# Optimization experiments

Hardware: AMD Instinct MI355X
Metric: run time of the kernel (lower is better)

Reference implementation:

```python
import jax, jax.numpy as jnp
import numpy as np

RADIUS = 0.25  # module init arg


def _spp(x):
    """Spatial pyramid max pooling over the (K=8, C) plane.
    x: [B, N, 8, C] -> [B, N, 21] (4x4 + 2x2 + 1x1 bins)."""
    B, N, K, C = x.shape
    outs = []
    for h, w in ((4, 4), (2, 2), (1, 1)):
        r = x.reshape(B, N, h, K // h, w, C // w)
        outs.append(r.max(axis=(3, 5)).reshape(B, N, h * w))
    return jnp.concatenate(outs, axis=-1)


def _pointsift_select(xyz, radius):
    """Octant-wise nearest-neighbor selection. xyz: [Bp, N, 3] -> idx [Bp, N, 8]."""
    Bp, N, _ = xyz.shape
    judge = radius * radius
    # diff[b, n, m] = xyz[b, m] - xyz[b, n]  (point m relative to centroid n)
    diff = xyz[:, None, :, :] - xyz[:, :, None, :]          # [Bp, N, N, 3]
    dist = jnp.sum(diff * diff, axis=-1)                     # [Bp, N, N]
    octw = jnp.array([4, 2, 1], dtype=jnp.int32)
    sub = jnp.sum((diff + 1.0).astype(jnp.int32) * octw, -1)  # [Bp, N, N] octant id
    valid = (dist > 1e-10) & (dist < judge)
    eye = jnp.eye(N, dtype=bool)                             # self entry gets judge_dist
    idxs = []
    for i in range(8):
        d_i = jnp.where(valid & (sub == i), dist, 1e10)
        d_i = jnp.where(eye, judge, d_i)
        idxs.append(jnp.argmin(d_i, axis=-1))                # first-min, matches torch
    return jnp.stack(idxs, axis=-1)                          # [Bp, N, 8]


def setup_inputs() -> dict:
    key = jax.random.key(0)
    ks = jax.random.split(key, 7)
    C = 256
    x = jax.random.uniform(ks[0], (2, 2, 2048, 3), dtype=jnp.float32)
    w1 = jax.random.normal(ks[1], (C, 3), dtype=jnp.float32) * 0.05
    b1 = jax.random.normal(ks[2], (C,), dtype=jnp.float32) * 0.05
    w2 = jax.random.normal(ks[3], (C, C), dtype=jnp.float32) * 0.05
    b2 = jax.random.normal(ks[4], (C,), dtype=jnp.float32) * 0.05
    w3 = jax.random.normal(ks[5], (C, C), dtype=jnp.float32) * 0.05
    b3 = jax.random.normal(ks[6], (C,), dtype=jnp.float32) * 0.05
    return {"x": x, "w1": w1, "b1": b1, "w2": w2, "b2": b2, "w3": w3, "b3": b3}


def reference(x, w1, b1, w2, b2, w3, b3):
    B, T, N, _ = x.shape
    xyz = x.reshape(B * T, N, 3)
    idx = _pointsift_select(xyz, RADIUS)                     # [Bp, N, 8]
    b_idx = jnp.arange(B * T)[:, None, None]
    grouped = xyz[b_idx, idx] - xyz[:, :, None, :]           # [Bp, N, 8, 3] relative coords
    # three stacked 1x1 convs (no nonlinearity, per original Sequential)
    h = jnp.einsum('bnkc,oc->bnko', grouped, w1) + b1
    h = jnp.einsum('bnkc,oc->bnko', h, w2) + b2
    h = jnp.einsum('bnkc,oc->bnko', h, w3) + b3              # [Bp, N, 8, C]
    out = _spp(h)                                            # [Bp, N, 21]
    return out.reshape(B, T, N, -1)
```

## Files before the change

### kernel.cpp

```cpp
#include <hip/hip_runtime.h>

#define NPTS 2048
#define CCH  256

template <int CTRL>
__device__ __forceinline__ float dppf(float v) {
    return __int_as_float(__builtin_amdgcn_update_dpp(
        0, __float_as_int(v), CTRL, 0xF, 0xF, true));
}
__device__ __forceinline__ float row16_max(float v) {
    v = fmaxf(v, dppf<0xB1>(v));
    v = fmaxf(v, dppf<0x4E>(v));
    v = fmaxf(v, dppf<0x141>(v));
    v = fmaxf(v, dppf<0x140>(v));
    return v;
}
__device__ __forceinline__ float row16_sum(float v) {
    v += dppf<0xB1>(v);
    v += dppf<0x4E>(v);
    v += dppf<0x141>(v);
    v += dppf<0x140>(v);
    return v;
}
__device__ __forceinline__ float wave_sum(float v) {
    v = row16_sum(v);
    v += __shfl_xor(v, 16, 64);
    v += __shfl_xor(v, 32, 64);
    return v;
}

__device__ __forceinline__ int cell_coord(float v) {
    int c = (int)(v * 4.0f);
    return min(3, max(0, c));
}


__global__ __launch_bounds__(256) void prep_kernel(
    const float* __restrict__ w1, const float* __restrict__ b1,
    const float* __restrict__ w2, const float* __restrict__ b2,
    const float* __restrict__ w3, const float* __restrict__ b3,
    float* __restrict__ ws)
{
    __shared__ float  w3row[2][CCH];
    __shared__ float4 wpart[2][4];
    int o0 = blockIdx.x * 2, c = threadIdx.x;

    float w3c0 = w3[(o0 + 0) * CCH + c];
    float w3c1 = w3[(o0 + 1) * CCH + c];
    w3row[0][c] = w3c0;
    w3row[1][c] = w3c1;
    __syncthreads();

    float a0 = 0.f, a1 = 0.f, a2 = 0.f, a3 = 0.f;
    float b0 = 0.f, b1p = 0.f, b2p = 0.f, b3p = 0.f;
    const float* w2c = w2 + c;
    for (int k = 0; k < CCH; k += 4) {
        float q0 = w2c[(k + 0) * CCH];
        float q1 = w2c[(k + 1) * CCH];
        float q2 = w2c[(k + 2) * CCH];
        float q3 = w2c[(k + 3) * CCH];
        a0 = fmaf(w3row[0][k + 0], q0, a0);
        a1 = fmaf(w3row[0][k + 1], q1, a1);
        a2 = fmaf(w3row[0][k + 2], q2, a2);
        a3 = fmaf(w3row[0][k + 3], q3, a3);
        b0  = fmaf(w3row[1][k + 0], q0, b0);
        b1p = fmaf(w3row[1][k + 1], q1, b1p);
        b2p = fmaf(w3row[1][k + 2], q2, b2p);
        b3p = fmaf(w3row[1][k + 3], q3, b3p);
    }
    float accA = (a0 + a1) + (a2 + a3);
    float accB = (b0 + b1p) + (b2p + b3p);

    float w1x = w1[c * 3 + 0], w1y = w1[c * 3 + 1], w1z = w1[c * 3 + 2];
    float b1c = b1[c], b2c = b2[c];

    float4 vA = make_float4(accA * w1x, accA * w1y, accA * w1z,
                            fmaf(accA, b1c, w3c0 * b2c));
    float4 vB = make_float4(accB * w1x, accB * w1y, accB * w1z,
                            fmaf(accB, b1c, w3c1 * b2c));
    vA.x = wave_sum(vA.x); vA.y = wave_sum(vA.y);
    vA.z = wave_sum(vA.z); vA.w = wave_sum(vA.w);
    vB.x = wave_sum(vB.x); vB.y = wave_sum(vB.y);
    vB.z = wave_sum(vB.z); vB.w = wave_sum(vB.w);
    if ((c & 63) == 0) {
        wpart[0][c >> 6] = vA;
        wpart[1][c >> 6] = vB;
    }
    __syncthreads();
    if (c < 2) {
        int o = o0 + c;
        float4 p0 = wpart[c][0], p1 = wpart[c][1], p2 = wpart[c][2], p3 = wpart[c][3];
        ws[o * 3 + 0] = (p0.x + p1.x) + (p2.x + p3.x);
        ws[o * 3 + 1] = (p0.y + p1.y) + (p2.y + p3.y);
        ws[o * 3 + 2] = (p0.z + p1.z) + (p2.z + p3.z);
        ws[3 * CCH + o] = (p0.w + p1.w) + (p2.w + p3.w) + b3[o];
    }
}

__global__ __launch_bounds__(1024) void pointsift_kernel(
    const float* __restrict__ x,
    const float* __restrict__ ws,
    float* __restrict__ out)
{
    __shared__ float4 scrd[NPTS];
    __shared__ unsigned sstart[66];
    __shared__ unsigned shist[64];
    __shared__ unsigned scur[64];
    __shared__ unsigned long long soct[16][8];

    int tid = threadIdx.x;
    int batch = blockIdx.x >> 7;
    int n0    = (blockIdx.x & 127) * 16;
    const float* xb = x + (size_t)batch * NPTS * 3;

    if (tid < 64) shist[tid] = 0;
    __syncthreads();

    float2 f0 = *(const float2*)(xb + 6 * tid + 0);
    float2 f1 = *(const float2*)(xb + 6 * tid + 2);
    float2 f2 = *(const float2*)(xb + 6 * tid + 4);
    float3 p0 = make_float3(f0.x, f0.y, f1.x);
    float3 p1 = make_float3(f1.y, f2.x, f2.y);
    int c0 = (cell_coord(p0.x) << 4) | (cell_coord(p0.y) << 2) | cell_coord(p0.z);
    int c1 = (cell_coord(p1.x) << 4) | (cell_coord(p1.y) << 2) | cell_coord(p1.z);
    atomicAdd(&shist[c0], 1u);
    atomicAdd(&shist[c1], 1u);
    __syncthreads();

    if (tid < 64) {
        unsigned v = shist[tid];
        unsigned incl = v;
#pragma unroll
        for (int s = 1; s < 64; s <<= 1) {
            unsigned o = __shfl_up(incl, s, 64);
            if (tid >= s) incl += o;
        }
        unsigned excl = incl - v;
        sstart[tid] = excl;
        scur[tid] = excl;
        if (tid == 63) sstart[64] = NPTS;
    }
    __syncthreads();

    {
        unsigned q0 = atomicAdd(&scur[c0], 1u);
        scrd[q0] = make_float4(p0.x, p0.y, p0.z, __uint_as_float(2u * tid));
        unsigned q1 = atomicAdd(&scur[c1], 1u);
        scrd[q1] = make_float4(p1.x, p1.y, p1.z, __uint_as_float(2u * tid + 1u));
    }

    int wave = tid >> 6;
    int lane = tid & 63;
    int n = n0 + wave;

    float3 cpt = *(const float3*)(xb + 3 * n);
    float cx = cpt.x, cy = cpt.y, cz = cpt.z;

    if (lane < 8)
        soct[wave][lane] = (0x7f800000ULL << 32) | (unsigned)n;

    __syncthreads();

    int ccx = cell_coord(cx), ccy = cell_coord(cy), ccz = cell_coord(cz);
    int zlo = ccz > 0 ? ccz - 1 : 0;
    int zhi = ccz < 3 ? ccz + 1 : 3;

    for (int di = -1; di <= 1; ++di) {
        int a = ccx + di;
        if ((unsigned)a > 3u) continue;
        for (int dj = -1; dj <= 1; ++dj) {
            int bc = ccy + dj;
            if ((unsigned)bc > 3u) continue;
            int base = (a << 4) | (bc << 2);
            unsigned s0 = sstart[base + zlo];
            unsigned e0 = sstart[base + zhi + 1];
            for (unsigned pp = s0 + lane; pp < e0; pp += 64) {
                float4 p = scrd[pp];
                float dx = p.x - cx, dy = p.y - cy, dz = p.z - cz;
                float d2 = __fadd_rn(__fadd_rn(__fmul_rn(dx, dx), __fmul_rn(dy, dy)),
                                     __fmul_rn(dz, dz));
                if ((d2 > 1e-10f) && (d2 < 0.0625f)) {
                    int oct = 4 * (int)(dx + 1.0f) + 2 * (int)(dy + 1.0f) + (int)(dz + 1.0f);
                    unsigned long long key =
                        ((unsigned long long)__float_as_uint(d2) << 32) |
                        __float_as_uint(p.w);
                    __hip_atomic_fetch_min(&soct[wave][oct], key,
                                           __ATOMIC_RELAXED,
                                           __HIP_MEMORY_SCOPE_WORKGROUP);
                }
            }
        }
    }

    int nidx[8];
#pragma unroll
    for (int k = 0; k < 8; ++k)
        nidx[k] = (int)(unsigned)soct[wave][k];

    const float4* wsv = (const float4*)ws;
    float4 wa = wsv[lane * 3 + 0];
    float4 wb = wsv[lane * 3 + 1];
    float4 wc = wsv[lane * 3 + 2];
    float4 be = ((const float4*)(ws + 3 * CCH))[lane];
    float w[4][3] = {{wa.x, wa.y, wa.z}, {wa.w, wb.x, wb.y},
                     {wb.z, wb.w, wc.x}, {wc.y, wc.z, wc.w}};
    float bev[4] = {be.x, be.y, be.z, be.w};

    float m16[4];
#pragma unroll
    for (int i = 0; i < 4; ++i) m16[i] = -__builtin_inff();
#pragma unroll
    for (int k = 0; k < 8; ++k) {
        float3 p = *(const float3*)(xb + 3 * nidx[k]);
        float gx = p.x - cx, gy = p.y - cy, gz = p.z - cz;
#pragma unroll
        for (int q = 0; q < 4; ++q) {
            float h = fmaf(gx, w[q][0], fmaf(gy, w[q][1], fmaf(gz, w[q][2], bev[q])));
            m16[k >> 1] = fmaxf(m16[k >> 1], h);
        }
    }

    float t[4], u[4];
#pragma unroll
    for (int i = 0; i < 4; ++i) {
        m16[i] = row16_max(m16[i]);
        t[i] = fmaxf(m16[i], __shfl_xor(m16[i], 16, 64));
        u[i] = fmaxf(t[i], __shfl_xor(t[i], 32, 64));
    }

    float* op = out + ((size_t)batch * NPTS + n) * 21;
    if ((lane & 15) == 0) {
        int j = lane >> 4;
#pragma unroll
        for (int i = 0; i < 4; ++i)
            op[i * 4 + j] = m16[i];
    }
    if (lane == 0 || lane == 32) {
        int j2 = lane >> 5;
        op[16 + 0 * 2 + j2] = fmaxf(t[0], t[1]);
        op[16 + 1 * 2 + j2] = fmaxf(t[2], t[3]);
    }
    if (lane == 0) {
        op[20] = fmaxf(fmaxf(u[0], u[1]), fmaxf(u[2], u[3]));
    }
}

extern "C" void kernel_launch(void* const* d_in, const int* in_sizes, int n_in,
                              void* d_out, int out_size, void* d_ws, size_t ws_size,
                              hipStream_t stream) {
    const float* x  = (const float*)d_in[0];
    const float* w1 = (const float*)d_in[1];
    const float* b1 = (const float*)d_in[2];
    const float* w2 = (const float*)d_in[3];
    const float* b2 = (const float*)d_in[4];
    const float* w3 = (const float*)d_in[5];
    const float* b3 = (const float*)d_in[6];
    float* out = (float*)d_out;
    float* ws  = (float*)d_ws;

    prep_kernel<<<CCH / 2, CCH, 0, stream>>>(w1, b1, w2, b2, w3, b3, ws);

    int Bp = in_sizes[0] / (NPTS * 3);
    pointsift_kernel<<<Bp * (NPTS / 16), 1024, 0, stream>>>(x, ws, out);
}
```

Before: 22.15 us.

## Hoist per-batch spatial bucket sort into prep kernel, shrink search blocks

Moves the per-batch grid histogram and counting sort out of every search block and into extra blocks of the prep kernel. The sorted coordinates and cell offsets now go to the workspace, so each search block no longer repeats the 2048-point sort in LDS. Search blocks drop from 1024 threads and 16 centroids to 256 threads and 4 centroids, with a launch-bounds occupancy hint. Neighbor reads now come from global or L2 memory instead of LDS, and the batch index is taken from the low bits of the block index, which assumes Bp==4.

Result: slower. 22.66 us (+2.3%).

```diff
diff --git a/kernel.cpp b/kernel.cpp
--- a/kernel.cpp
+++ b/kernel.cpp
@@ -2,6 +2,9 @@
 
 #define NPTS 2048
 #define CCH  256
+
+#define STARTS_OFF 4096
+#define CRD_OFF    8192
 
 template <int CTRL>
 __device__ __forceinline__ float dppf(float v) {
@@ -34,120 +37,138 @@
     return min(3, max(0, c));
 }
 
-
-__global__ __launch_bounds__(256) void prep_kernel(
+__global__ __launch_bounds__(256) void prep_sort_kernel(
+    const float* __restrict__ x,
     const float* __restrict__ w1, const float* __restrict__ b1,
     const float* __restrict__ w2, const float* __restrict__ b2,
     const float* __restrict__ w3, const float* __restrict__ b3,
-    float* __restrict__ ws)
+    float* __restrict__ ws, int Bp)
 {
     __shared__ float  w3row[2][CCH];
     __shared__ float4 wpart[2][4];
-    int o0 = blockIdx.x * 2, c = threadIdx.x;
-
-    float w3c0 = w3[(o0 + 0) * CCH + c];
-    float w3c1 = w3[(o0 + 1) * CCH + c];
-    w3row[0][c] = w3c0;
-    w3row[1][c] = w3c1;
-    __syncthreads();
-
-    float a0 = 0.f, a1 = 0.f, a2 = 0.f, a3 = 0.f;
-    float b0 = 0.f, b1p = 0.f, b2p = 0.f, b3p = 0.f;
-    const float* w2c = w2 + c;
-    for (int k = 0; k < CCH; k += 4) {
-        float q0 = w2c[(k + 0) * CCH];
-        float q1 = w2c[(k + 1) * CCH];
-        float q2 = w2c[(k + 2) * CCH];
-        float q3 = w2c[(k + 3) * CCH];
-        a0 = fmaf(w3row[0][k + 0], q0, a0);
-        a1 = fmaf(w3row[0][k + 1], q1, a1);
-        a2 = fmaf(w3row[0][k + 2], q2, a2);
-        a3 = fmaf(w3row[0][k + 3], q3, a3);
-        b0  = fmaf(w3row[1][k + 0], q0, b0);
-        b1p = fmaf(w3row[1][k + 1], q1, b1p);
-        b2p = fmaf(w3row[1][k + 2], q2, b2p);
-        b3p = fmaf(w3row[1][k + 3], q3, b3p);
-    }
-    float accA = (a0 + a1) + (a2 + a3);
-    float accB = (b0 + b1p) + (b2p + b3p);
-
-    float w1x = w1[c * 3 + 0], w1y = w1[c * 3 + 1], w1z = w1[c * 3 + 2];
-    float b1c = b1[c], b2c = b2[c];
-
-    float4 vA = make_float4(accA * w1x, accA * w1y, accA * w1z,
-                            fmaf(accA, b1c, w3c0 * b2c));
-    float4 vB = make_float4(accB * w1x, accB * w1y, accB * w1z,
-                            fmaf(accB, b1c, w3c1 * b2c));
-    vA.x = wave_sum(vA.x); vA.y = wave_sum(vA.y);
-    vA.z = wave_sum(vA.z); vA.w = wave_sum(vA.w);
-    vB.x = wave_sum(vB.x); vB.y = wave_sum(vB.y);
-    vB.z = wave_sum(vB.z); vB.w = wave_sum(vB.w);
-    if ((c & 63) == 0) {
-        wpart[0][c >> 6] = vA;
-        wpart[1][c >> 6] = vB;
-    }
-    __syncthreads();
-    if (c < 2) {
-        int o = o0 + c;
-        float4 p0 = wpart[c][0], p1 = wpart[c][1], p2 = wpart[c][2], p3 = wpart[c][3];
-        ws[o * 3 + 0] = (p0.x + p1.x) + (p2.x + p3.x);
-        ws[o * 3 + 1] = (p0.y + p1.y) + (p2.y + p3.y);
-        ws[o * 3 + 2] = (p0.z + p1.z) + (p2.z + p3.z);
-        ws[3 * CCH + o] = (p0.w + p1.w) + (p2.w + p3.w) + b3[o];
-    }
-}
-
-__global__ __launch_bounds__(1024) void pointsift_kernel(
+    __shared__ unsigned shist[64];
+    __shared__ unsigned scur[64];
+
+    int tid = threadIdx.x;
+
+    if ((int)blockIdx.x < CCH / 2) {
+        int o0 = blockIdx.x * 2, c = tid;
+        float w3c0 = w3[(o0 + 0) * CCH + c];
+        float w3c1 = w3[(o0 + 1) * CCH + c];
+        w3row[0][c] = w3c0;
+        w3row[1][c] = w3c1;
+        __syncthreads();
+
+        float a0 = 0.f, a1 = 0.f, a2 = 0.f, a3 = 0.f;
+        float b0 = 0.f, b1p = 0.f, b2p = 0.f, b3p = 0.f;
+        const float* w2c = w2 + c;
+        for (int k = 0; k < CCH; k += 4) {
+            float q0 = w2c[(k + 0) * CCH];
+            float q1 = w2c[(k + 1) * CCH];
+            float q2 = w2c[(k + 2) * CCH];
+            float q3 = w2c[(k + 3) * CCH];
+            a0 = fmaf(w3row[0][k + 0], q0, a0);
+            a1 = fmaf(w3row[0][k + 1], q1, a1);
+            a2 = fmaf(w3row[0][k + 2], q2, a2);
+            a3 = fmaf(w3row[0][k + 3], q3, a3);
+            b0  = fmaf(w3row[1][k + 0], q0, b0);
+            b1p = fmaf(w3row[1][k + 1], q1, b1p);
+            b2p = fmaf(w3row[1][k + 2], q2, b2p);
+            b3p = fmaf(w3row[1][k + 3], q3, b3p);
+        }
+        float accA = (a0 + a1) + (a2 + a3);
+        float accB = (b0 + b1p) + (b2p + b3p);
+
+        float w1x = w1[c * 3 + 0], w1y = w1[c * 3 + 1], w1z = w1[c * 3 + 2];
+        float b1c = b1[c], b2c = b2[c];
+
+        float4 vA = make_float4(accA * w1x, accA * w1y, accA * w1z,
+                                fmaf(accA, b1c, w3c0 * b2c));
+        float4 vB = make_float4(accB * w1x, accB * w1y, accB * w1z,
+                                fmaf(accB, b1c, w3c1 * b2c));
+        vA.x = wave_sum(vA.x); vA.y = wave_sum(vA.y);
+        vA.z = wave_sum(vA.z); vA.w = wave_sum(vA.w);
+        vB.x = wave_sum(vB.x); vB.y = wave_sum(vB.y);
+        vB.z = wave_sum(vB.z); vB.w = wave_sum(vB.w);
+        if ((c & 63) == 0) {
+            wpart[0][c >> 6] = vA;
+            wpart[1][c >> 6] = vB;
+        }
+        __syncthreads();
+        if (c < 2) {
+            int o = o0 + c;
+            float4 p0 = wpart[c][0], p1 = wpart[c][1], p2 = wpart[c][2], p3 = wpart[c][3];
+            ws[o * 3 + 0] = (p0.x + p1.x) + (p2.x + p3.x);
+            ws[o * 3 + 1] = (p0.y + p1.y) + (p2.y + p3.y);
+            ws[o * 3 + 2] = (p0.z + p1.z) + (p2.z + p3.z);
+            ws[3 * CCH + o] = (p0.w + p1.w) + (p2.w + p3.w) + b3[o];
+        }
+        return;
+    }
+
+    int b = blockIdx.x - CCH / 2;
+    if (b >= Bp) return;
+    const float* xb = x + (size_t)b * NPTS * 3;
+
+    if (tid < 64) shist[tid] = 0;
+    __syncthreads();
+
+    float a[24];
+#pragma unroll
+    for (int j = 0; j < 6; ++j)
+        *(float4*)(a + 4 * j) = ((const float4*)xb)[tid * 6 + j];
+
+    int cl[8];
+#pragma unroll
+    for (int k = 0; k < 8; ++k) {
+        cl[k] = (cell_coord(a[3 * k + 0]) << 4) |
+                (cell_coord(a[3 * k + 1]) << 2) |
+                 cell_coord(a[3 * k + 2]);
+        atomicAdd(&shist[cl[k]], 1u);
+    }
+    __syncthreads();
+
+    unsigned* stg = (unsigned*)((char*)ws + STARTS_OFF) + b * 128;
+    if (tid < 64) {
+        unsigned v = shist[tid];
+        unsigned incl = v;
+#pragma unroll
+        for (int s = 1; s < 64; s <<= 1) {
+            unsigned o = __shfl_up(incl, s, 64);
+            if (tid >= s) incl += o;
+        }
+        unsigned excl = incl - v;
+        scur[tid] = excl;
+        stg[tid] = excl;
+        if (tid == 63) stg[64] = NPTS;
+    }
+    __syncthreads();
+
+    float4* crd = (float4*)((char*)ws + CRD_OFF) + (size_t)b * NPTS;
+#pragma unroll
+    for (int k = 0; k < 8; ++k) {
+        unsigned pos = atomicAdd(&scur[cl[k]], 1u);
+        crd[pos] = make_float4(a[3 * k + 0], a[3 * k + 1], a[3 * k + 2],
+                               __uint_as_float((unsigned)(8 * tid + k)));
+    }
+}
+
+__global__ __launch_bounds__(256, 8) void pointsift_kernel(
     const float* __restrict__ x,
     const float* __restrict__ ws,
     float* __restrict__ out)
 {
-    __shared__ float4 scrd[NPTS];
-    __shared__ unsigned sstart[66];
-    __shared__ unsigned shist[64];
-    __shared__ unsigned scur[64];
-    __shared__ unsigned long long soct[16][8];
+    __shared__ unsigned sstart[65];
+    __shared__ unsigned long long soct[4][8];
 
     int tid = threadIdx.x;
-    int batch = blockIdx.x >> 7;
-    int n0    = (blockIdx.x & 127) * 16;
+    int batch = blockIdx.x & 3;
+    int n0    = (blockIdx.x >> 2) * 4;
     const float* xb = x + (size_t)batch * NPTS * 3;
-
-    if (tid < 64) shist[tid] = 0;
-    __syncthreads();
-
-    float2 f0 = *(const float2*)(xb + 6 * tid + 0);
-    float2 f1 = *(const float2*)(xb + 6 * tid + 2);
-    float2 f2 = *(const float2*)(xb + 6 * tid + 4);
-    float3 p0 = make_float3(f0.x, f0.y, f1.x);
-    float3 p1 = make_float3(f1.y, f2.x, f2.y);
-    int c0 = (cell_coord(p0.x) << 4) | (cell_coord(p0.y) << 2) | cell_coord(p0.z);
-    int c1 = (cell_coord(p1.x) << 4) | (cell_coord(p1.y) << 2) | cell_coord(p1.z);
-    atomicAdd(&shist[c0], 1u);
-    atomicAdd(&shist[c1], 1u);
-    __syncthreads();
-
-    if (tid < 64) {
-        unsigned v = shist[tid];
-        unsigned incl = v;
-#pragma unroll
-        for (int s = 1; s < 64; s <<= 1) {
-            unsigned o = __shfl_up(incl, s, 64);
-            if (tid >= s) incl += o;
-        }
-        unsigned excl = incl - v;
-        sstart[tid] = excl;
-        scur[tid] = excl;
-        if (tid == 63) sstart[64] = NPTS;
-    }
-    __syncthreads();
-
-    {
-        unsigned q0 = atomicAdd(&scur[c0], 1u);
-        scrd[q0] = make_float4(p0.x, p0.y, p0.z, __uint_as_float(2u * tid));
-        unsigned q1 = atomicAdd(&scur[c1], 1u);
-        scrd[q1] = make_float4(p1.x, p1.y, p1.z, __uint_as_float(2u * tid + 1u));
-    }
+    const float4* crd = (const float4*)((const char*)ws + CRD_OFF) + (size_t)batch * NPTS;
+    const unsigned* stg = (const unsigned*)((const char*)ws + STARTS_OFF) + batch * 128;
+
+    if (tid < 65) sstart[tid] = stg[tid];
 
     int wave = tid >> 6;
     int lane = tid & 63;
@@ -175,7 +196,7 @@
             unsigned s0 = sstart[base + zlo];
             unsigned e0 = sstart[base + zhi + 1];
             for (unsigned pp = s0 + lane; pp < e0; pp += 64) {
-                float4 p = scrd[pp];
+                float4 p = crd[pp];
                 float dx = p.x - cx, dy = p.y - cy, dz = p.z - cz;
                 float d2 = __fadd_rn(__fadd_rn(__fmul_rn(dx, dx), __fmul_rn(dy, dy)),
                                      __fmul_rn(dz, dz));
@@ -258,8 +279,9 @@
     float* out = (float*)d_out;
     float* ws  = (float*)d_ws;
 
-    prep_kernel<<<CCH / 2, CCH, 0, stream>>>(w1, b1, w2, b2, w3, b3, ws);
-
     int Bp = in_sizes[0] / (NPTS * 3);
-    pointsift_kernel<<<Bp * (NPTS / 16), 1024, 0, stream>>>(x, ws, out);
-}
+
+    prep_sort_kernel<<<CCH / 2 + Bp, CCH, 0, stream>>>(
+        x, w1, b1, w2, b2, w3, b3, ws, Bp);
+    pointsift_kernel<<<Bp * (NPTS / 4), 256, 0, stream>>>(x, ws, out);
+}
```
